# Optimization experiments

Measured on AMD Instinct MI355X. Metric: run time of the kernel, lower is better.

Reference implementation:

```python
import jax, jax.numpy as jnp
import numpy as np

N_NODES = 100000
N_EDGES = 1600000
N_GRAPHS = 256
SEQ = 365
F_DYN = 16
F_STAT = 32
H_GNN = 64
H_RNN = 128
EPS = 1e-5  # BatchNorm eps (eval mode, running stats)


def _bn(x, g, b, m, v):
    return (x - m) * jax.lax.rsqrt(v + EPS) * g + b


def _gcn(x, src, dst, W, b, n):
    # PyG GCNConv: linear -> sym-normalized aggregation with self-loops -> bias
    h = x @ W  # [n, out]
    deg = jnp.ones((n,), h.dtype).at[dst].add(1.0)  # in-degree + self-loop
    dinv = jax.lax.rsqrt(deg)
    norm = dinv[src] * dinv[dst]  # [E]
    agg = jnp.zeros_like(h).at[dst].add(h[src] * norm[:, None])
    agg = agg + h * (dinv * dinv)[:, None]  # self-loop contribution
    return agg + b


def _lstm_layer(x, Wih, Whh, bih, bhh):
    # torch nn.LSTM gate order: i, f, g, o; Wih [4H, in], Whh [4H, H]
    B = x.shape[0]
    H = Whh.shape[1]
    def step(carry, xt):
        h, c = carry
        z = xt @ Wih.T + h @ Whh.T + bih + bhh
        i, f, g, o = jnp.split(z, 4, axis=-1)
        c = jax.nn.sigmoid(f) * c + jax.nn.sigmoid(i) * jnp.tanh(g)
        h = jax.nn.sigmoid(o) * jnp.tanh(c)
        return (h, c), h
    init = (jnp.zeros((B, H), x.dtype), jnp.zeros((B, H), x.dtype))
    _, hs = jax.lax.scan(step, init, jnp.swapaxes(x, 0, 1))
    return jnp.swapaxes(hs, 0, 1)


def setup_inputs() -> dict:
    key = jax.random.key(0)
    ks = jax.random.split(key, 40)
    def rn(i, shape, scale=1.0):
        return jax.random.normal(ks[i], shape, jnp.float32) * scale
    inp = {}
    inp['dynamic_features'] = rn(0, (N_GRAPHS, SEQ, F_DYN))
    inp['x_static'] = rn(1, (N_NODES, F_STAT))
    inp['edge_index'] = jax.random.randint(ks[2], (2, N_EDGES), 0, N_NODES, jnp.int32)
    inp['batch_idx'] = jnp.sort(jax.random.randint(ks[3], (N_NODES,), 0, N_GRAPHS, jnp.int32))
    # GCN weights stored [in, out] (equivalent to torch [out, in] transposed)
    inp['W_g1'] = rn(4, (F_STAT, H_GNN), F_STAT ** -0.5)
    inp['b_g1'] = jnp.zeros((H_GNN,), jnp.float32)
    inp['W_g2'] = rn(5, (H_GNN, H_GNN), H_GNN ** -0.5)
    inp['b_g2'] = jnp.zeros((H_GNN,), jnp.float32)
    for i, name in [(6, 'bn1'), (7, 'bn2')]:
        inp[name + '_gamma'] = jnp.ones((H_GNN,), jnp.float32)
        inp[name + '_beta'] = jnp.zeros((H_GNN,), jnp.float32)
        inp[name + '_mean'] = rn(i, (H_GNN,), 0.1)
        inp[name + '_var'] = jax.random.uniform(ks[i + 10], (H_GNN,), jnp.float32) + 0.5
    G = 4 * H_RNN
    inp['lstm0_Wih'] = rn(8, (G, F_DYN), F_DYN ** -0.5)
    inp['lstm0_Whh'] = rn(9, (G, H_RNN), H_RNN ** -0.5)
    inp['lstm0_bih'] = jnp.zeros((G,), jnp.float32)
    inp['lstm0_bhh'] = jnp.zeros((G,), jnp.float32)
    inp['lstm1_Wih'] = rn(20, (G, H_RNN), H_RNN ** -0.5)
    inp['lstm1_Whh'] = rn(21, (G, H_RNN), H_RNN ** -0.5)
    inp['lstm1_bih'] = jnp.zeros((G,), jnp.float32)
    inp['lstm1_bhh'] = jnp.zeros((G,), jnp.float32)
    F_FUSE = H_GNN + H_RNN
    inp['W_f1'] = rn(22, (F_FUSE, 128), F_FUSE ** -0.5)
    inp['b_f1'] = jnp.zeros((128,), jnp.float32)
    inp['fbn_gamma'] = jnp.ones((128,), jnp.float32)
    inp['fbn_beta'] = jnp.zeros((128,), jnp.float32)
    inp['fbn_mean'] = rn(23, (128,), 0.1)
    inp['fbn_var'] = jax.random.uniform(ks[24], (128,), jnp.float32) + 0.5
    inp['W_f2'] = rn(25, (128, 64), 128 ** -0.5)
    inp['b_f2'] = jnp.zeros((64,), jnp.float32)
    inp['W_out'] = rn(26, (64, 10), 64 ** -0.5)
    inp['b_out'] = jnp.zeros((10,), jnp.float32)
    return inp


def reference(dynamic_features, x_static, edge_index, batch_idx,
              W_g1, b_g1, W_g2, b_g2,
              bn1_gamma, bn1_beta, bn1_mean, bn1_var,
              bn2_gamma, bn2_beta, bn2_mean, bn2_var,
              lstm0_Wih, lstm0_Whh, lstm0_bih, lstm0_bhh,
              lstm1_Wih, lstm1_Whh, lstm1_bih, lstm1_bhh,
              W_f1, b_f1, fbn_gamma, fbn_beta, fbn_mean, fbn_var,
              W_f2, b_f2, W_out, b_out):
    src, dst = edge_index[0], edge_index[1]
    n = x_static.shape[0]
    # GNN branch (dropout is identity in eval)
    h = jax.nn.relu(_bn(_gcn(x_static, src, dst, W_g1, b_g1, n), bn1_gamma, bn1_beta, bn1_mean, bn1_var))
    h = jax.nn.relu(_bn(_gcn(h, src, dst, W_g2, b_g2, n), bn2_gamma, bn2_beta, bn2_mean, bn2_var))
    # global mean pool over graphs
    sums = jax.ops.segment_sum(h, batch_idx, num_segments=N_GRAPHS)
    cnt = jax.ops.segment_sum(jnp.ones((n,), h.dtype), batch_idx, num_segments=N_GRAPHS)
    gnn_emb = sums / jnp.maximum(cnt, 1.0)[:, None]
    # RNN branch: 2-layer LSTM, take last timestep
    r = _lstm_layer(dynamic_features, lstm0_Wih, lstm0_Whh, lstm0_bih, lstm0_bhh)
    r = _lstm_layer(r, lstm1_Wih, lstm1_Whh, lstm1_bih, lstm1_bhh)
    rnn_emb = r[:, -1, :]
    # Fusion head
    fused = jnp.concatenate([gnn_emb, rnn_emb], axis=1)
    x = jax.nn.relu(_bn(fused @ W_f1 + b_f1, fbn_gamma, fbn_beta, fbn_mean, fbn_var))
    x = jax.nn.relu(x @ W_f2 + b_f2)
    return x @ W_out + b_out
```

## Files before the change

### kernel.cpp

```cpp
#include <hip/hip_runtime.h>

#define N_NODES 100000
#define N_EDGES 1600000
#define N_GRAPHS 256
#define SEQ 365
#define F_DYN 16
#define H_GNN 64
#define GATES 512
#define EPSV 1e-5f
#define TC 48
#define NCHUNK 8
#define NBLK_SCAN 391

__device__ __forceinline__ float rl(float v, int l) {
    return __int_as_float(__builtin_amdgcn_readlane(__float_as_int(v), l));
}
__device__ __forceinline__ float sigmoidf_(float x) { return 1.f / (1.f + __expf(-x)); }
__device__ __forceinline__ float tanhf_(float x) { return 1.f - 2.f / (__expf(2.f * x) + 1.f); }


__global__ void hist_kernel(const int* __restrict__ ei, int* __restrict__ deg) {
    int e = blockIdx.x * 256 + threadIdx.x;
    if (e < N_EDGES) atomicAdd(&deg[ei[N_EDGES + e]], 1);
}

__global__ __launch_bounds__(256) void scan1_kernel(const int* __restrict__ deg, int* __restrict__ bsum) {
    __shared__ int sm[256];
    int n = blockIdx.x * 256 + threadIdx.x;
    sm[threadIdx.x] = (n < N_NODES) ? deg[n] : 0;
    __syncthreads();
    for (int off = 128; off > 0; off >>= 1) {
        if (threadIdx.x < off) sm[threadIdx.x] += sm[threadIdx.x + off];
        __syncthreads();
    }
    if (threadIdx.x == 0) bsum[blockIdx.x] = sm[0];
}

__global__ __launch_bounds__(512) void scan2_kernel(int* __restrict__ bsum) {
    __shared__ int sc[512];
    int tid = threadIdx.x;
    int v = (tid < NBLK_SCAN) ? bsum[tid] : 0;
    sc[tid] = v;
    __syncthreads();
    for (int off = 1; off < 512; off <<= 1) {
        int t = (tid >= off) ? sc[tid - off] : 0;
        __syncthreads();
        sc[tid] += t;
        __syncthreads();
    }
    if (tid < NBLK_SCAN) bsum[tid] = sc[tid] - v;
}

__global__ __launch_bounds__(256) void scan3_kernel(const int* __restrict__ deg, const int* __restrict__ bsum,
                                                    int* __restrict__ offs, int* __restrict__ cursor,
                                                    float* __restrict__ dinv) {
    __shared__ int sc[256];
    int tid = threadIdx.x, n = blockIdx.x * 256 + tid;
    int v = (n < N_NODES) ? deg[n] : 0;
    sc[tid] = v;
    __syncthreads();
    for (int off = 1; off < 256; off <<= 1) {
        int t = (tid >= off) ? sc[tid - off] : 0;
        __syncthreads();
        sc[tid] += t;
        __syncthreads();
    }
    int ex = sc[tid] - v + bsum[blockIdx.x];
    if (n < N_NODES) {
        offs[n] = ex;
        cursor[n] = ex;
        dinv[n] = rsqrtf(1.f + (float)v);
        if (n == N_NODES - 1) offs[N_NODES] = ex + v;
    }
}

__global__ void fill_kernel(const int* __restrict__ ei, const float* __restrict__ dinv,
                            int* __restrict__ cursor, int2* __restrict__ epk) {
    int e = blockIdx.x * 256 + threadIdx.x;
    if (e >= N_EDGES) return;
    int s = ei[e], d = ei[N_EDGES + e];
    int pos = atomicAdd(&cursor[d], 1);
    epk[pos] = make_int2(s, __float_as_int(dinv[s] * dinv[d]));
}


template <int K>
__global__ __launch_bounds__(256) void mm_kernel(const float* __restrict__ X,
                                                 const float* __restrict__ W,
                                                 float* __restrict__ P) {
    __shared__ float Xs[64 * K];
    __shared__ float Ws[K * 64];
    int tid = threadIdx.x, bm = blockIdx.x;
#pragma unroll
    for (int i = 0; i < (K * 64 / 4) / 256; i++)
        ((float4*)Ws)[i * 256 + tid] = ((const float4*)W)[i * 256 + tid];
#pragma unroll
    for (int i = 0; i < (64 * K / 4) / 256; i++) {
        int f4 = i * 256 + tid;
        int r = (f4 * 4) / K, c = (f4 * 4) % K;
        int row = bm * 64 + r;
        float4 v = make_float4(0.f, 0.f, 0.f, 0.f);
        if (row < N_NODES) v = *(const float4*)(X + (size_t)row * K + c);
        ((float4*)Xs)[f4] = v;
    }
    __syncthreads();
    int f = tid & 63, nz = tid >> 6;
    float acc[16];
#pragma unroll
    for (int i = 0; i < 16; i++) acc[i] = 0.f;
    for (int k = 0; k < K; k++) {
        float wv = Ws[k * 64 + f];
#pragma unroll
        for (int ni = 0; ni < 16; ni++) acc[ni] += Xs[(nz * 16 + ni) * K + k] * wv;
    }
#pragma unroll
    for (int ni = 0; ni < 16; ni++) {
        int row = bm * 64 + nz * 16 + ni;
        if (row < N_NODES) P[(size_t)row * 64 + f] = acc[ni];
    }
}

__global__ __launch_bounds__(256) void gather_kernel(const float* __restrict__ P,
                                                     const int2* __restrict__ epk,
                                                     const int* __restrict__ offs,
                                                     const float* __restrict__ dinv,
                                                     const float* __restrict__ bias,
                                                     const float* __restrict__ gm, const float* __restrict__ bt,
                                                     const float* __restrict__ mn, const float* __restrict__ vr,
                                                     float* __restrict__ H) {
    int node = blockIdx.x * 4 + (threadIdx.x >> 6);
    int f = threadIdx.x & 63;
    float di = dinv[node];
    int beg = offs[node], end = offs[node + 1];
    float acc0 = P[(size_t)node * 64 + f] * di * di;
    float acc1 = 0.f;
    int i = beg;
    for (; i + 1 < end; i += 2) {
        int2 e0 = epk[i], e1 = epk[i + 1];
        acc0 += P[(size_t)e0.x * 64 + f] * __int_as_float(e0.y);
        acc1 += P[(size_t)e1.x * 64 + f] * __int_as_float(e1.y);
    }
    if (i < end) {
        int2 e0 = epk[i];
        acc0 += P[(size_t)e0.x * 64 + f] * __int_as_float(e0.y);
    }
    float vv = acc0 + acc1 + bias[f];
    float s = gm[f] * rsqrtf(vr[f] + EPSV);
    vv = (vv - mn[f]) * s + bt[f];
    H[(size_t)node * 64 + f] = fmaxf(vv, 0.f);
}

__global__ __launch_bounds__(256) void pool_kernel(const float* __restrict__ H,
                                                   const int* __restrict__ batch,
                                                   float* __restrict__ emb) {
    int g = blockIdx.x, tid = threadIdx.x;
    int lo = 0, hi = N_NODES;
    while (lo < hi) { int mid = (lo + hi) >> 1; if (batch[mid] < g) lo = mid + 1; else hi = mid; }
    int start = lo;
    hi = N_NODES;
    while (lo < hi) { int mid = (lo + hi) >> 1; if (batch[mid] < g + 1) lo = mid + 1; else hi = mid; }
    int end = lo;
    int f = tid & 63, p = tid >> 6;
    float acc = 0.f;
    for (int n = start + p; n < end; n += 4) acc += H[(size_t)n * 64 + f];
    __shared__ float sm[4][64];
    sm[p][f] = acc;
    __syncthreads();
    if (p == 0) {
        float tot = sm[0][f] + sm[1][f] + sm[2][f] + sm[3][f];
        emb[g * 64 + f] = tot / fmaxf((float)(end - start), 1.f);
    }
}


__global__ __launch_bounds__(512, 2) void lstm0_kernel(const float* __restrict__ dyn,
                                                       const float* __restrict__ Wih,
                                                       const float* __restrict__ Whh,
                                                       const float* __restrict__ bih,
                                                       const float* __restrict__ bhh,
                                                       float* __restrict__ H0) {
    int b = blockIdx.x, g = threadIdx.x, lane = g & 63;
    float w[128];
    const float4* W4 = (const float4*)(Whh + (size_t)g * 128);
#pragma unroll
    for (int i = 0; i < 32; i++) {
        float4 v = W4[i];
        w[4 * i] = v.x; w[4 * i + 1] = v.y; w[4 * i + 2] = v.z; w[4 * i + 3] = v.w;
    }
    float wx[16];
    const float4* Wx4 = (const float4*)(Wih + (size_t)g * 16);
#pragma unroll
    for (int i = 0; i < 4; i++) {
        float4 v = Wx4[i];
        wx[4 * i] = v.x; wx[4 * i + 1] = v.y; wx[4 * i + 2] = v.z; wx[4 * i + 3] = v.w;
    }
    float bias = bih[g] + bhh[g];
    __shared__ float h_s[128];
    __shared__ float z_s[512];
    float c = 0.f;
    if (g < 128) h_s[g] = 0.f;
    __syncthreads();
    const float* xb = dyn + (size_t)b * SEQ * F_DYN;
    float* Hb = H0 + (size_t)b * SEQ * 128;
    float xtv = xb[lane & 15];
    for (int t = 0; t < SEQ; t++) {
        float xtn = (t + 1 < SEQ) ? xb[(t + 1) * 16 + (lane & 15)] : 0.f;
        float hva = h_s[lane], hvb = h_s[64 + lane];
        float a0 = bias, a1 = 0.f, a2 = 0.f, a3 = 0.f;
#pragma unroll
        for (int k = 0; k < 16; k += 4) {
            a0 += wx[k] * rl(xtv, k);
            a1 += wx[k + 1] * rl(xtv, k + 1);
            a2 += wx[k + 2] * rl(xtv, k + 2);
            a3 += wx[k + 3] * rl(xtv, k + 3);
        }
#pragma unroll
        for (int k = 0; k < 64; k += 4) {
            a0 += w[k] * rl(hva, k);
            a1 += w[k + 1] * rl(hva, k + 1);
            a2 += w[k + 2] * rl(hva, k + 2);
            a3 += w[k + 3] * rl(hva, k + 3);
        }
#pragma unroll
        for (int k = 0; k < 64; k += 4) {
            a0 += w[64 + k] * rl(hvb, k);
            a1 += w[65 + k] * rl(hvb, k + 1);
            a2 += w[66 + k] * rl(hvb, k + 2);
            a3 += w[67 + k] * rl(hvb, k + 3);
        }
        z_s[g] = (a0 + a1) + (a2 + a3);
        __syncthreads();
        if (g < 128) {
            float zi = z_s[g], zf = z_s[g + 128], zg = z_s[g + 256], zo = z_s[g + 384];
            float ii = sigmoidf_(zi), ff = sigmoidf_(zf), gg = tanhf_(zg), oo = sigmoidf_(zo);
            c = ff * c + ii * gg;
            float hn = oo * tanhf_(c);
            h_s[g] = hn;
            Hb[t * 128 + g] = hn;
        }
        __syncthreads();
        xtv = xtn;
    }
}

__global__ __launch_bounds__(256, 2) void gemm_a1_kernel(const float* __restrict__ H0,
                                                         const float* __restrict__ B,
                                                         const float* __restrict__ bih,
                                                         const float* __restrict__ bhh,
                                                         float* __restrict__ A1c, int t0) {
    __shared__ float As[64][132];
    __shared__ float Bs[64][132];
    int tid = threadIdx.x;
    int bm = blockIdx.x, bn = blockIdx.y;
    int tx = tid & 15, ty = tid >> 4;
    float acc[8][8];
#pragma unroll
    for (int i = 0; i < 8; i++)
#pragma unroll
        for (int j = 0; j < 8; j++) acc[i][j] = 0.f;
    for (int kc = 0; kc < 128; kc += 64) {
#pragma unroll
        for (int i = 0; i < 8; i++) {
            int f4 = i * 256 + tid;
            int r = f4 >> 4;
            int cc = (f4 & 15) * 4;
            int row = bm * 128 + r;
            int bb = row / TC, tl = row - bb * TC;
            int t = t0 + tl;
            float4 v = make_float4(0.f, 0.f, 0.f, 0.f);
            if (t < SEQ) v = *(const float4*)(H0 + ((size_t)bb * SEQ + t) * 128 + kc + cc);
            As[cc + 0][r] = v.x; As[cc + 1][r] = v.y; As[cc + 2][r] = v.z; As[cc + 3][r] = v.w;
            float4 u = *(const float4*)(B + (size_t)(bn * 128 + r) * 128 + kc + cc);
            Bs[cc + 0][r] = u.x; Bs[cc + 1][r] = u.y; Bs[cc + 2][r] = u.z; Bs[cc + 3][r] = u.w;
        }
        __syncthreads();
#pragma unroll
        for (int k = 0; k < 64; k++) {
            float av[8], bv[8];
            *(float4*)&av[0] = *(const float4*)&As[k][ty * 8];
            *(float4*)&av[4] = *(const float4*)&As[k][ty * 8 + 4];
            *(float4*)&bv[0] = *(const float4*)&Bs[k][tx * 8];
            *(float4*)&bv[4] = *(const float4*)&Bs[k][tx * 8 + 4];
#pragma unroll
            for (int i = 0; i < 8; i++)
#pragma unroll
                for (int j = 0; j < 8; j++) acc[i][j] += av[i] * bv[j];
        }
        __syncthreads();
    }
    float bb8[8];
#pragma unroll
    for (int j = 0; j < 8; j++) {
        int col = bn * 128 + tx * 8 + j;
        bb8[j] = bih[col] + bhh[col];
    }
#pragma unroll
    for (int i = 0; i < 8; i++) {
        int row = bm * 128 + ty * 8 + i;
        float4 o0 = make_float4(acc[i][0] + bb8[0], acc[i][1] + bb8[1], acc[i][2] + bb8[2], acc[i][3] + bb8[3]);
        float4 o1 = make_float4(acc[i][4] + bb8[4], acc[i][5] + bb8[5], acc[i][6] + bb8[6], acc[i][7] + bb8[7]);
        *(float4*)(A1c + (size_t)row * GATES + bn * 128 + tx * 8) = o0;
        *(float4*)(A1c + (size_t)row * GATES + bn * 128 + tx * 8 + 4) = o1;
    }
}

__global__ __launch_bounds__(512, 2) void lstm1_kernel(const float* __restrict__ A1c,
                                                       const float* __restrict__ Whh,
                                                       float* __restrict__ state,
                                                       float* __restrict__ rnn, int t0, int tc) {
    int b = blockIdx.x, g = threadIdx.x, lane = g & 63;
    float w[128];
    const float4* W4 = (const float4*)(Whh + (size_t)g * 128);
#pragma unroll
    for (int i = 0; i < 32; i++) {
        float4 v = W4[i];
        w[4 * i] = v.x; w[4 * i + 1] = v.y; w[4 * i + 2] = v.z; w[4 * i + 3] = v.w;
    }
    __shared__ float h_s[128];
    __shared__ float z_s[512];
    float c = 0.f;
    if (g < 128) {
        if (t0 == 0) {
            h_s[g] = 0.f;
        } else {
            h_s[g] = state[b * 128 + g];
            c = state[N_GRAPHS * 128 + b * 128 + g];
        }
    }
    __syncthreads();
    const float* Ab = A1c + (size_t)b * TC * GATES;
    float a_cur = Ab[g];
    float hn = 0.f;
    for (int tl = 0; tl < tc; tl++) {
        float a_next = (tl + 1 < tc) ? Ab[(tl + 1) * GATES + g] : 0.f;
        float hva = h_s[lane], hvb = h_s[64 + lane];
        float a0 = a_cur, a1 = 0.f, a2 = 0.f, a3 = 0.f;
#pragma unroll
        for (int k = 0; k < 64; k += 4) {
            a0 += w[k] * rl(hva, k);
            a1 += w[k + 1] * rl(hva, k + 1);
            a2 += w[k + 2] * rl(hva, k + 2);
            a3 += w[k + 3] * rl(hva, k + 3);
        }
#pragma unroll
        for (int k = 0; k < 64; k += 4) {
            a0 += w[64 + k] * rl(hvb, k);
            a1 += w[65 + k] * rl(hvb, k + 1);
            a2 += w[66 + k] * rl(hvb, k + 2);
            a3 += w[67 + k] * rl(hvb, k + 3);
        }
        z_s[g] = (a0 + a1) + (a2 + a3);
        __syncthreads();
        if (g < 128) {
            float zi = z_s[g], zf = z_s[g + 128], zg = z_s[g + 256], zo = z_s[g + 384];
            float ii = sigmoidf_(zi), ff = sigmoidf_(zf), gg = tanhf_(zg), oo = sigmoidf_(zo);
            c = ff * c + ii * gg;
            hn = oo * tanhf_(c);
            h_s[g] = hn;
        }
        __syncthreads();
        a_cur = a_next;
    }
    if (g < 128) {
        state[b * 128 + g] = hn;
        state[N_GRAPHS * 128 + b * 128 + g] = c;
        if (t0 + tc == SEQ) rnn[b * 128 + g] = hn;
    }
}


__global__ __launch_bounds__(128) void head_kernel(const float* __restrict__ gnn, const float* __restrict__ rnn,
                                                   const float* __restrict__ Wf1, const float* __restrict__ bf1,
                                                   const float* __restrict__ fg, const float* __restrict__ fb,
                                                   const float* __restrict__ fm, const float* __restrict__ fv,
                                                   const float* __restrict__ Wf2, const float* __restrict__ bf2,
                                                   const float* __restrict__ Wo, const float* __restrict__ bo,
                                                   float* __restrict__ out) {
    int b = blockIdx.x, tid = threadIdx.x;
    __shared__ float fused[192];
    __shared__ float x1[128];
    __shared__ float x2[64];
    if (tid < 64) fused[tid] = gnn[b * 64 + tid];
    fused[64 + tid] = rnn[b * 128 + tid];
    __syncthreads();
    float acc = bf1[tid];
    for (int k = 0; k < 192; k++) acc += fused[k] * Wf1[k * 128 + tid];
    float s = fg[tid] * rsqrtf(fv[tid] + EPSV);
    acc = (acc - fm[tid]) * s + fb[tid];
    x1[tid] = fmaxf(acc, 0.f);
    __syncthreads();
    if (tid < 64) {
        float a2 = bf2[tid];
        for (int k = 0; k < 128; k++) a2 += x1[k] * Wf2[k * 64 + tid];
        x2[tid] = fmaxf(a2, 0.f);
    }
    __syncthreads();
    if (tid < 10) {
        float a3 = bo[tid];
        for (int k = 0; k < 64; k++) a3 += x2[k] * Wo[k * 10 + tid];
        out[b * 10 + tid] = a3;
    }
}

extern "C" void kernel_launch(void* const* d_in, const int* in_sizes, int n_in,
                              void* d_out, int out_size, void* d_ws, size_t ws_size,
                              hipStream_t stream) {
    const float* dyn = (const float*)d_in[0];
    const float* xs = (const float*)d_in[1];
    const int* ei = (const int*)d_in[2];
    const int* batch = (const int*)d_in[3];
    const float* Wg1 = (const float*)d_in[4];
    const float* bg1 = (const float*)d_in[5];
    const float* Wg2 = (const float*)d_in[6];
    const float* bg2 = (const float*)d_in[7];
    const float* bn1g = (const float*)d_in[8], *bn1b = (const float*)d_in[9];
    const float* bn1m = (const float*)d_in[10], *bn1v = (const float*)d_in[11];
    const float* bn2g = (const float*)d_in[12], *bn2b = (const float*)d_in[13];
    const float* bn2m = (const float*)d_in[14], *bn2v = (const float*)d_in[15];
    const float* l0Wih = (const float*)d_in[16], *l0Whh = (const float*)d_in[17];
    const float* l0bih = (const float*)d_in[18], *l0bhh = (const float*)d_in[19];
    const float* l1Wih = (const float*)d_in[20], *l1Whh = (const float*)d_in[21];
    const float* l1bih = (const float*)d_in[22], *l1bhh = (const float*)d_in[23];
    const float* Wf1 = (const float*)d_in[24], *bf1 = (const float*)d_in[25];
    const float* fbg = (const float*)d_in[26], *fbb = (const float*)d_in[27];
    const float* fbm = (const float*)d_in[28], *fbv = (const float*)d_in[29];
    const float* Wf2 = (const float*)d_in[30], *bf2 = (const float*)d_in[31];
    const float* Wo = (const float*)d_in[32], *bo = (const float*)d_in[33];
    float* out = (float*)d_out;

    float* ws = (float*)d_ws;
    float* P = ws;
    float* H = P + 6400000;
    float* dinv = H + 6400000;
    float* gnn = dinv + 100000;
    float* rnn = gnn + 16384;
    float* st = rnn + 32768;
    float* H0 = st + 65536;
    float* A1c = H0 + 11962880;
    int* deg = (int*)(A1c + 6291456);
    int* offs = deg + 100096;
    int* cursor = offs + 100001;
    int* bsum = cursor + 100001;
    int2* epk = (int2*)(bsum + 512);

    hipMemsetAsync(deg, 0, N_NODES * sizeof(int), stream);
    hist_kernel<<<(N_EDGES + 255) / 256, 256, 0, stream>>>(ei, deg);
    scan1_kernel<<<NBLK_SCAN, 256, 0, stream>>>(deg, bsum);
    scan2_kernel<<<1, 512, 0, stream>>>(bsum);
    scan3_kernel<<<NBLK_SCAN, 256, 0, stream>>>(deg, bsum, offs, cursor, dinv);
    fill_kernel<<<(N_EDGES + 255) / 256, 256, 0, stream>>>(ei, dinv, cursor, epk);

    mm_kernel<32><<<(N_NODES + 63) / 64, 256, 0, stream>>>(xs, Wg1, P);
    gather_kernel<<<N_NODES / 4, 256, 0, stream>>>(P, epk, offs, dinv, bg1, bn1g, bn1b, bn1m, bn1v, H);
    mm_kernel<64><<<(N_NODES + 63) / 64, 256, 0, stream>>>(H, Wg2, P);
    gather_kernel<<<N_NODES / 4, 256, 0, stream>>>(P, epk, offs, dinv, bg2, bn2g, bn2b, bn2m, bn2v, H);

    pool_kernel<<<N_GRAPHS, 256, 0, stream>>>(H, batch, gnn);

    lstm0_kernel<<<N_GRAPHS, 512, 0, stream>>>(dyn, l0Wih, l0Whh, l0bih, l0bhh, H0);
    for (int ch = 0; ch < NCHUNK; ch++) {
        int t0 = ch * TC;
        int tc = (SEQ - t0 < TC) ? (SEQ - t0) : TC;
        gemm_a1_kernel<<<dim3(96, 4), 256, 0, stream>>>(H0, l1Wih, l1bih, l1bhh, A1c, t0);
        lstm1_kernel<<<N_GRAPHS, 512, 0, stream>>>(A1c, l1Whh, st, rnn, t0, tc);
    }

    head_kernel<<<N_GRAPHS, 128, 0, stream>>>(gnn, rnn, Wf1, bf1, fbg, fbb, fbm, fbv, Wf2, bf2, Wo, bo, out);
}
```

Measured before the change: 1.835 ms.

## Pipeline LSTM layers across streams and overlap GCN branch concurrently

Splits the layer-0 LSTM into time chunks that save and restore their h/c state, so each chunk's input-projection GEMM and layer-1 LSTM can run on separate streams while later layer-0 chunks proceed. A double-buffered A1 workspace with event dependencies lets layer 1 trail layer 0 by one chunk. The GCN branch moves to its own stream so it runs concurrently with the recurrent work. The cost is more kernel launches and weight reloads per chunk, plus heavier reliance on the LSTM kernels actually co-residing on the GPU.

```diff
diff --git a/kernel.cpp b/kernel.cpp
--- a/kernel.cpp
+++ b/kernel.cpp
@@ -8,8 +8,9 @@
 #define H_GNN 64
 #define GATES 512
 #define EPSV 1e-5f
-#define TC 48
-#define NCHUNK 8
+#define TC 32
+#define NCHUNK 12
+#define A1ELEMS (N_GRAPHS * TC * GATES)
 #define NBLK_SCAN 391
 
 __device__ __forceinline__ float rl(float v, int l) {
@@ -17,6 +18,26 @@
 }
 __device__ __forceinline__ float sigmoidf_(float x) { return 1.f / (1.f + __expf(-x)); }
 __device__ __forceinline__ float tanhf_(float x) { return 1.f - 2.f / (__expf(2.f * x) + 1.f); }
+
+static hipStream_t s_gcn = nullptr, s_gemm = nullptr, s_l1 = nullptr;
+static hipEvent_t evFork = nullptr, evGCN = nullptr;
+static hipEvent_t evC0[NCHUNK], evG[NCHUNK], evL[NCHUNK];
+static bool g_ok = false;
+static struct SideInit {
+    SideInit() {
+        g_ok = true;
+        if (hipStreamCreateWithFlags(&s_gcn, hipStreamNonBlocking) != hipSuccess) g_ok = false;
+        if (hipStreamCreateWithFlags(&s_gemm, hipStreamNonBlocking) != hipSuccess) g_ok = false;
+        if (hipStreamCreateWithFlags(&s_l1, hipStreamNonBlocking) != hipSuccess) g_ok = false;
+        if (hipEventCreateWithFlags(&evFork, hipEventDisableTiming) != hipSuccess) g_ok = false;
+        if (hipEventCreateWithFlags(&evGCN, hipEventDisableTiming) != hipSuccess) g_ok = false;
+        for (int i = 0; i < NCHUNK; i++) {
+            if (hipEventCreateWithFlags(&evC0[i], hipEventDisableTiming) != hipSuccess) g_ok = false;
+            if (hipEventCreateWithFlags(&evG[i], hipEventDisableTiming) != hipSuccess) g_ok = false;
+            if (hipEventCreateWithFlags(&evL[i], hipEventDisableTiming) != hipSuccess) g_ok = false;
+        }
+    }
+} s_side_init;
 
 
 __global__ void hist_kernel(const int* __restrict__ ei, int* __restrict__ deg) {
@@ -173,12 +194,14 @@
 }
 
 
-__global__ __launch_bounds__(512, 2) void lstm0_kernel(const float* __restrict__ dyn,
-                                                       const float* __restrict__ Wih,
-                                                       const float* __restrict__ Whh,
-                                                       const float* __restrict__ bih,
-                                                       const float* __restrict__ bhh,
-                                                       float* __restrict__ H0) {
+__global__ __launch_bounds__(512, 2) void lstm0c_kernel(const float* __restrict__ dyn,
+                                                        const float* __restrict__ Wih,
+                                                        const float* __restrict__ Whh,
+                                                        const float* __restrict__ bih,
+                                                        const float* __restrict__ bhh,
+                                                        float* __restrict__ H0,
+                                                        float* __restrict__ l0st,
+                                                        int t0, int tc) {
     int b = blockIdx.x, g = threadIdx.x, lane = g & 63;
     float w[128];
     const float4* W4 = (const float4*)(Whh + (size_t)g * 128);
@@ -198,12 +221,21 @@
     __shared__ float h_s[128];
     __shared__ float z_s[512];
     float c = 0.f;
-    if (g < 128) h_s[g] = 0.f;
+    if (g < 128) {
+        if (t0 == 0) {
+            h_s[g] = 0.f;
+        } else {
+            h_s[g] = l0st[b * 128 + g];
+            c = l0st[N_GRAPHS * 128 + b * 128 + g];
+        }
+    }
     __syncthreads();
     const float* xb = dyn + (size_t)b * SEQ * F_DYN;
     float* Hb = H0 + (size_t)b * SEQ * 128;
-    float xtv = xb[lane & 15];
-    for (int t = 0; t < SEQ; t++) {
+    float xtv = xb[t0 * 16 + (lane & 15)];
+    float hn = 0.f;
+    for (int tl = 0; tl < tc; tl++) {
+        int t = t0 + tl;
         float xtn = (t + 1 < SEQ) ? xb[(t + 1) * 16 + (lane & 15)] : 0.f;
         float hva = h_s[lane], hvb = h_s[64 + lane];
         float a0 = bias, a1 = 0.f, a2 = 0.f, a3 = 0.f;
@@ -234,12 +266,16 @@
             float zi = z_s[g], zf = z_s[g + 128], zg = z_s[g + 256], zo = z_s[g + 384];
             float ii = sigmoidf_(zi), ff = sigmoidf_(zf), gg = tanhf_(zg), oo = sigmoidf_(zo);
             c = ff * c + ii * gg;
-            float hn = oo * tanhf_(c);
+            hn = oo * tanhf_(c);
             h_s[g] = hn;
             Hb[t * 128 + g] = hn;
         }
         __syncthreads();
         xtv = xtn;
+    }
+    if (g < 128) {
+        l0st[b * 128 + g] = hn;
+        l0st[N_GRAPHS * 128 + b * 128 + g] = c;
     }
 }
 
@@ -265,7 +301,7 @@
             int r = f4 >> 4;
             int cc = (f4 & 15) * 4;
             int row = bm * 128 + r;
-            int bb = row / TC, tl = row - bb * TC;
+            int bb = row >> 5, tl = row & (TC - 1);
             int t = t0 + tl;
             float4 v = make_float4(0.f, 0.f, 0.f, 0.f);
             if (t < SEQ) v = *(const float4*)(H0 + ((size_t)bb * SEQ + t) * 128 + kc + cc);
@@ -435,34 +471,67 @@
     float* gnn = dinv + 100000;
     float* rnn = gnn + 16384;
     float* st = rnn + 32768;
-    float* H0 = st + 65536;
-    float* A1c = H0 + 11962880;
-    int* deg = (int*)(A1c + 6291456);
+    float* l0st = st + 65536;
+    float* H0 = l0st + 65536;
+    float* A1a = H0 + 11962880;
+    float* A1b = A1a + A1ELEMS;
+    int* deg = (int*)(A1b + A1ELEMS);
     int* offs = deg + 100096;
     int* cursor = offs + 100001;
     int* bsum = cursor + 100001;
     int2* epk = (int2*)(bsum + 512);
 
-    hipMemsetAsync(deg, 0, N_NODES * sizeof(int), stream);
-    hist_kernel<<<(N_EDGES + 255) / 256, 256, 0, stream>>>(ei, deg);
-    scan1_kernel<<<NBLK_SCAN, 256, 0, stream>>>(deg, bsum);
-    scan2_kernel<<<1, 512, 0, stream>>>(bsum);
-    scan3_kernel<<<NBLK_SCAN, 256, 0, stream>>>(deg, bsum, offs, cursor, dinv);
-    fill_kernel<<<(N_EDGES + 255) / 256, 256, 0, stream>>>(ei, dinv, cursor, epk);
-
-    mm_kernel<32><<<(N_NODES + 63) / 64, 256, 0, stream>>>(xs, Wg1, P);
-    gather_kernel<<<N_NODES / 4, 256, 0, stream>>>(P, epk, offs, dinv, bg1, bn1g, bn1b, bn1m, bn1v, H);
-    mm_kernel<64><<<(N_NODES + 63) / 64, 256, 0, stream>>>(H, Wg2, P);
-    gather_kernel<<<N_NODES / 4, 256, 0, stream>>>(P, epk, offs, dinv, bg2, bn2g, bn2b, bn2m, bn2v, H);
-
-    pool_kernel<<<N_GRAPHS, 256, 0, stream>>>(H, batch, gnn);
-
-    lstm0_kernel<<<N_GRAPHS, 512, 0, stream>>>(dyn, l0Wih, l0Whh, l0bih, l0bhh, H0);
-    for (int ch = 0; ch < NCHUNK; ch++) {
-        int t0 = ch * TC;
-        int tc = (SEQ - t0 < TC) ? (SEQ - t0) : TC;
-        gemm_a1_kernel<<<dim3(96, 4), 256, 0, stream>>>(H0, l1Wih, l1bih, l1bhh, A1c, t0);
-        lstm1_kernel<<<N_GRAPHS, 512, 0, stream>>>(A1c, l1Whh, st, rnn, t0, tc);
+    float* A1buf[2] = {A1a, A1b};
+    bool MS = g_ok && s_gcn && s_gemm && s_l1;
+
+    hipStream_t sg = MS ? s_gcn : stream;
+    hipStream_t sm = MS ? s_gemm : stream;
+    hipStream_t sl = MS ? s_l1 : stream;
+
+    if (MS) {
+        hipEventRecord(evFork, stream);
+        hipStreamWaitEvent(sg, evFork, 0);
+    }
+
+    hipMemsetAsync(deg, 0, N_NODES * sizeof(int), sg);
+    hist_kernel<<<(N_EDGES + 255) / 256, 256, 0, sg>>>(ei, deg);
+    scan1_kernel<<<NBLK_SCAN, 256, 0, sg>>>(deg, bsum);
+    scan2_kernel<<<1, 512, 0, sg>>>(bsum);
+    scan3_kernel<<<NBLK_SCAN, 256, 0, sg>>>(deg, bsum, offs, cursor, dinv);
+    fill_kernel<<<(N_EDGES + 255) / 256, 256, 0, sg>>>(ei, dinv, cursor, epk);
+    mm_kernel<32><<<(N_NODES + 63) / 64, 256, 0, sg>>>(xs, Wg1, P);
+    gather_kernel<<<N_NODES / 4, 256, 0, sg>>>(P, epk, offs, dinv, bg1, bn1g, bn1b, bn1m, bn1v, H);
+    mm_kernel<64><<<(N_NODES + 63) / 64, 256, 0, sg>>>(H, Wg2, P);
+    gather_kernel<<<N_NODES / 4, 256, 0, sg>>>(P, epk, offs, dinv, bg2, bn2g, bn2b, bn2m, bn2v, H);
+    pool_kernel<<<N_GRAPHS, 256, 0, sg>>>(H, batch, gnn);
+    if (MS) hipEventRecord(evGCN, sg);
+
+    if (MS) {
+        for (int ch = 0; ch < NCHUNK; ch++) {
+            int t0 = ch * TC;
+            int tc = (SEQ - t0 < TC) ? (SEQ - t0) : TC;
+            lstm0c_kernel<<<N_GRAPHS, 512, 0, stream>>>(dyn, l0Wih, l0Whh, l0bih, l0bhh, H0, l0st, t0, tc);
+            hipEventRecord(evC0[ch], stream);
+
+            hipStreamWaitEvent(sm, evC0[ch], 0);
+            if (ch >= 2) hipStreamWaitEvent(sm, evL[ch - 2], 0);
+            gemm_a1_kernel<<<dim3(64, 4), 256, 0, sm>>>(H0, l1Wih, l1bih, l1bhh, A1buf[ch & 1], t0);
+            hipEventRecord(evG[ch], sm);
+
+            hipStreamWaitEvent(sl, evG[ch], 0);
+            lstm1_kernel<<<N_GRAPHS, 512, 0, sl>>>(A1buf[ch & 1], l1Whh, st, rnn, t0, tc);
+            hipEventRecord(evL[ch], sl);
+        }
+        hipStreamWaitEvent(stream, evL[NCHUNK - 1], 0);
+        hipStreamWaitEvent(stream, evGCN, 0);
+    } else {
+        for (int ch = 0; ch < NCHUNK; ch++) {
+            int t0 = ch * TC;
+            int tc = (SEQ - t0 < TC) ? (SEQ - t0) : TC;
+            lstm0c_kernel<<<N_GRAPHS, 512, 0, stream>>>(dyn, l0Wih, l0Whh, l0bih, l0bhh, H0, l0st, t0, tc);
+            gemm_a1_kernel<<<dim3(64, 4), 256, 0, stream>>>(H0, l1Wih, l1bih, l1bhh, A1buf[ch & 1], t0);
+            lstm1_kernel<<<N_GRAPHS, 512, 0, stream>>>(A1buf[ch & 1], l1Whh, st, rnn, t0, tc);
+        }
     }
 
     head_kernel<<<N_GRAPHS, 128, 0, stream>>>(gnn, rnn, Wf1, bf1, fbg, fbb, fbm, fbv, Wf2, bf2, Wo, bo, out);
```

New measurement: 2.170 ms. 18.2% more time.

## Run GCN branch on side stream concurrently with LSTM layer 0

Applied to the files above, without the earlier changes.

Moves the whole GCN pipeline (degree histogram, CSR build, two GCN layers, pooling) onto a separate non-blocking stream. A fork event starts it and a join event syncs it back, so it can run while the serial LSTM layer-0 recurrence occupies the main stream. The layer-1 input-projection GEMM is retiled to 512 threads with 4x8 outputs per thread, and its output alternates between two buffers, one reusing the GCN scratch area. This adds stream and event setup in a static initializer, and it relies on the GCN kernels finding spare compute units while lstm0 runs.

```diff
diff --git a/kernel.cpp b/kernel.cpp
--- a/kernel.cpp
+++ b/kernel.cpp
@@ -10,6 +10,7 @@
 #define EPSV 1e-5f
 #define TC 48
 #define NCHUNK 8
+#define A1ELEMS (N_GRAPHS * TC * GATES)
 #define NBLK_SCAN 391
 
 __device__ __forceinline__ float rl(float v, int l) {
@@ -17,6 +18,18 @@
 }
 __device__ __forceinline__ float sigmoidf_(float x) { return 1.f / (1.f + __expf(-x)); }
 __device__ __forceinline__ float tanhf_(float x) { return 1.f - 2.f / (__expf(2.f * x) + 1.f); }
+
+static hipStream_t s_gcn = nullptr;
+static hipEvent_t evFork = nullptr, evGCN = nullptr;
+static bool g_ok = false;
+static struct SideInit {
+    SideInit() {
+        g_ok = true;
+        if (hipStreamCreateWithFlags(&s_gcn, hipStreamNonBlocking) != hipSuccess) g_ok = false;
+        if (hipEventCreateWithFlags(&evFork, hipEventDisableTiming) != hipSuccess) g_ok = false;
+        if (hipEventCreateWithFlags(&evGCN, hipEventDisableTiming) != hipSuccess) g_ok = false;
+    }
+} s_side_init;
 
 
 __global__ void hist_kernel(const int* __restrict__ ei, int* __restrict__ deg) {
@@ -243,25 +256,25 @@
     }
 }
 
-__global__ __launch_bounds__(256, 2) void gemm_a1_kernel(const float* __restrict__ H0,
-                                                         const float* __restrict__ B,
-                                                         const float* __restrict__ bih,
-                                                         const float* __restrict__ bhh,
-                                                         float* __restrict__ A1c, int t0) {
+__global__ __launch_bounds__(512) void gemm_a1_kernel(const float* __restrict__ H0,
+                                                      const float* __restrict__ B,
+                                                      const float* __restrict__ bih,
+                                                      const float* __restrict__ bhh,
+                                                      float* __restrict__ A1c, int t0) {
     __shared__ float As[64][132];
     __shared__ float Bs[64][132];
     int tid = threadIdx.x;
     int bm = blockIdx.x, bn = blockIdx.y;
     int tx = tid & 15, ty = tid >> 4;
-    float acc[8][8];
-#pragma unroll
-    for (int i = 0; i < 8; i++)
+    float acc[4][8];
+#pragma unroll
+    for (int i = 0; i < 4; i++)
 #pragma unroll
         for (int j = 0; j < 8; j++) acc[i][j] = 0.f;
     for (int kc = 0; kc < 128; kc += 64) {
 #pragma unroll
-        for (int i = 0; i < 8; i++) {
-            int f4 = i * 256 + tid;
+        for (int i = 0; i < 4; i++) {
+            int f4 = i * 512 + tid;
             int r = f4 >> 4;
             int cc = (f4 & 15) * 4;
             int row = bm * 128 + r;
@@ -276,13 +289,12 @@
         __syncthreads();
 #pragma unroll
         for (int k = 0; k < 64; k++) {
-            float av[8], bv[8];
-            *(float4*)&av[0] = *(const float4*)&As[k][ty * 8];
-            *(float4*)&av[4] = *(const float4*)&As[k][ty * 8 + 4];
+            float av[4], bv[8];
+            *(float4*)&av[0] = *(const float4*)&As[k][ty * 4];
             *(float4*)&bv[0] = *(const float4*)&Bs[k][tx * 8];
             *(float4*)&bv[4] = *(const float4*)&Bs[k][tx * 8 + 4];
 #pragma unroll
-            for (int i = 0; i < 8; i++)
+            for (int i = 0; i < 4; i++)
 #pragma unroll
                 for (int j = 0; j < 8; j++) acc[i][j] += av[i] * bv[j];
         }
@@ -295,8 +307,8 @@
         bb8[j] = bih[col] + bhh[col];
     }
 #pragma unroll
-    for (int i = 0; i < 8; i++) {
-        int row = bm * 128 + ty * 8 + i;
+    for (int i = 0; i < 4; i++) {
+        int row = bm * 128 + ty * 4 + i;
         float4 o0 = make_float4(acc[i][0] + bb8[0], acc[i][1] + bb8[1], acc[i][2] + bb8[2], acc[i][3] + bb8[3]);
         float4 o1 = make_float4(acc[i][4] + bb8[4], acc[i][5] + bb8[5], acc[i][6] + bb8[6], acc[i][7] + bb8[7]);
         *(float4*)(A1c + (size_t)row * GATES + bn * 128 + tx * 8) = o0;
@@ -436,33 +448,43 @@
     float* rnn = gnn + 16384;
     float* st = rnn + 32768;
     float* H0 = st + 65536;
-    float* A1c = H0 + 11962880;
-    int* deg = (int*)(A1c + 6291456);
+    float* A1a = H0 + 11962880;
+    int* deg = (int*)(A1a + A1ELEMS);
     int* offs = deg + 100096;
     int* cursor = offs + 100001;
     int* bsum = cursor + 100001;
     int2* epk = (int2*)(bsum + 512);
-
-    hipMemsetAsync(deg, 0, N_NODES * sizeof(int), stream);
-    hist_kernel<<<(N_EDGES + 255) / 256, 256, 0, stream>>>(ei, deg);
-    scan1_kernel<<<NBLK_SCAN, 256, 0, stream>>>(deg, bsum);
-    scan2_kernel<<<1, 512, 0, stream>>>(bsum);
-    scan3_kernel<<<NBLK_SCAN, 256, 0, stream>>>(deg, bsum, offs, cursor, dinv);
-    fill_kernel<<<(N_EDGES + 255) / 256, 256, 0, stream>>>(ei, dinv, cursor, epk);
-
-    mm_kernel<32><<<(N_NODES + 63) / 64, 256, 0, stream>>>(xs, Wg1, P);
-    gather_kernel<<<N_NODES / 4, 256, 0, stream>>>(P, epk, offs, dinv, bg1, bn1g, bn1b, bn1m, bn1v, H);
-    mm_kernel<64><<<(N_NODES + 63) / 64, 256, 0, stream>>>(H, Wg2, P);
-    gather_kernel<<<N_NODES / 4, 256, 0, stream>>>(P, epk, offs, dinv, bg2, bn2g, bn2b, bn2m, bn2v, H);
-
-    pool_kernel<<<N_GRAPHS, 256, 0, stream>>>(H, batch, gnn);
+    float* A1b = P;
+
+    float* A1buf[2] = {A1a, A1b};
+    bool MS = g_ok && s_gcn;
+    hipStream_t sg = MS ? s_gcn : stream;
+
+    if (MS) {
+        hipEventRecord(evFork, stream);
+        hipStreamWaitEvent(sg, evFork, 0);
+    }
+
+    hipMemsetAsync(deg, 0, N_NODES * sizeof(int), sg);
+    hist_kernel<<<(N_EDGES + 255) / 256, 256, 0, sg>>>(ei, deg);
+    scan1_kernel<<<NBLK_SCAN, 256, 0, sg>>>(deg, bsum);
+    scan2_kernel<<<1, 512, 0, sg>>>(bsum);
+    scan3_kernel<<<NBLK_SCAN, 256, 0, sg>>>(deg, bsum, offs, cursor, dinv);
+    fill_kernel<<<(N_EDGES + 255) / 256, 256, 0, sg>>>(ei, dinv, cursor, epk);
+    mm_kernel<32><<<(N_NODES + 63) / 64, 256, 0, sg>>>(xs, Wg1, P);
+    gather_kernel<<<N_NODES / 4, 256, 0, sg>>>(P, epk, offs, dinv, bg1, bn1g, bn1b, bn1m, bn1v, H);
+    mm_kernel<64><<<(N_NODES + 63) / 64, 256, 0, sg>>>(H, Wg2, P);
+    gather_kernel<<<N_NODES / 4, 256, 0, sg>>>(P, epk, offs, dinv, bg2, bn2g, bn2b, bn2m, bn2v, H);
+    pool_kernel<<<N_GRAPHS, 256, 0, sg>>>(H, batch, gnn);
+    if (MS) hipEventRecord(evGCN, sg);
 
     lstm0_kernel<<<N_GRAPHS, 512, 0, stream>>>(dyn, l0Wih, l0Whh, l0bih, l0bhh, H0);
+    if (MS) hipStreamWaitEvent(stream, evGCN, 0);
     for (int ch = 0; ch < NCHUNK; ch++) {
         int t0 = ch * TC;
         int tc = (SEQ - t0 < TC) ? (SEQ - t0) : TC;
-        gemm_a1_kernel<<<dim3(96, 4), 256, 0, stream>>>(H0, l1Wih, l1bih, l1bhh, A1c, t0);
-        lstm1_kernel<<<N_GRAPHS, 512, 0, stream>>>(A1c, l1Whh, st, rnn, t0, tc);
+        gemm_a1_kernel<<<dim3(96, 4), 512, 0, stream>>>(H0, l1Wih, l1bih, l1bhh, A1buf[ch & 1], t0);
+        lstm1_kernel<<<N_GRAPHS, 512, 0, stream>>>(A1buf[ch & 1], l1Whh, st, rnn, t0, tc);
     }
 
     head_kernel<<<N_GRAPHS, 128, 0, stream>>>(gnn, rnn, Wf1, bf1, fbg, fbb, fbm, fbv, Wf2, bf2, Wo, bo, out);
```

After: 1.938 ms. 1.06x slower.
